# Kernel tuning notes

Measured on AMD Instinct MI355X. Metric: run time of the kernel, lower is better.

The kernel has to match this reference:

```python
import jax, jax.numpy as jnp
import numpy as np

BATCH, N, M, DIM, HID = 4, 2048, 2048, 128, 128
TB = 64  # target block size (mirrors the torch blocked loop, bounds the ijh intermediate)


def setup_inputs() -> dict:
    key = jax.random.key(0)
    k0, k1, k2, k3, k4, k5 = jax.random.split(key, 6)
    s_in = 1.0 / np.sqrt(DIM)
    s_out = 1.0 / np.sqrt(HID)
    return {
        "target_val": jax.random.normal(k0, (BATCH, N, DIM), jnp.float32),
        "source_val": jax.random.normal(k1, (BATCH, M, DIM), jnp.float32),
        "W_in": jax.random.uniform(k2, (HID, DIM), jnp.float32, -s_in, s_in),
        "b_in": jax.random.uniform(k3, (HID,), jnp.float32, -s_in, s_in),
        "W_out": jax.random.uniform(k4, (1, HID), jnp.float32, -s_out, s_out),
        "b_out": jax.random.uniform(k5, (1,), jnp.float32, -s_out, s_out),
    }


def reference(target_val, source_val, W_in, b_in, W_out, b_out):
    # out[b,i,j] = W_out @ silu(W_in @ (t_i * s_j) + b_in) + b_out
    B, Nt, d = target_val.shape
    nb = Nt // TB
    w_out = W_out[0]  # [HID]
    # [nb, B, TB, d] so we can scan over target blocks without materializing [B,N,M,HID]
    t_blocks = target_val.reshape(B, nb, TB, d).transpose(1, 0, 2, 3)

    def block_fn(t_chunk):  # t_chunk: [B, TB, d]
        hidden = jnp.einsum('bid,hd,bjd->bijh', t_chunk, W_in, source_val)  # [B,TB,M,HID]
        hidden = jax.nn.silu(hidden + b_in)
        return jnp.einsum('bijh,h->bij', hidden, w_out) + b_out[0]  # [B,TB,M]

    out_blocks = jax.lax.map(block_fn, t_blocks)  # [nb, B, TB, M]
    return out_blocks.transpose(1, 0, 2, 3).reshape(B, Nt, M)
```

## Files before the change

### kernel.cpp

```cpp
#include <hip/hip_runtime.h>

#define BATCH 4
#define NN 2048
#define MM 2048
#define DIM 128
#define HID 128

typedef __bf16 bf16x8 __attribute__((ext_vector_type(8)));
typedef float f32x16 __attribute__((ext_vector_type(16)));
typedef float f32x4 __attribute__((ext_vector_type(4)));
typedef float f32x2 __attribute__((ext_vector_type(2)));
typedef unsigned short ushort_t;
typedef ushort_t ushort8 __attribute__((ext_vector_type(8)));
typedef unsigned int uint_t;

#define LOG2E 1.44269504088896340736f
#define LN2   0.69314718055994530942f

__device__ __forceinline__ ushort_t f2bf(float f) {
  uint_t u = __builtin_bit_cast(uint_t, f);
  u += 0x7fffu + ((u >> 16) & 1u);
  return (ushort_t)(u >> 16);
}
__device__ __forceinline__ float bflo(uint_t p) { return __builtin_bit_cast(float, p << 16); }
__device__ __forceinline__ float bfhi(uint_t p) { return __builtin_bit_cast(float, p & 0xffff0000u); }

__global__ void cvt_repack(const float* __restrict__ src, ushort_t* __restrict__ dst) {
  int t = blockIdx.x * 256 + threadIdx.x;
  int c    = t & 63;
  int ks   = (t >> 6) & 7;
  int jt   = (t >> 9) & 63;
  int b    = t >> 15;
  int half = c >> 5, l5 = c & 31;
  int j    = jt * 32 + l5;
  int d0   = ks * 16 + half * 8;
  const float* s = src + ((size_t)(b * MM + j)) * DIM + d0;
  float4 v0 = *reinterpret_cast<const float4*>(s);
  float4 v1 = *reinterpret_cast<const float4*>(s + 4);
  ushort8 u;
  u[0] = f2bf(v0.x); u[1] = f2bf(v0.y); u[2] = f2bf(v0.z); u[3] = f2bf(v0.w);
  u[4] = f2bf(v1.x); u[5] = f2bf(v1.y); u[6] = f2bf(v1.z); u[7] = f2bf(v1.w);
  *reinterpret_cast<ushort8*>(dst + (size_t)t * 8) = u;
}

__global__ void pbw_kernel(const float* __restrict__ b_in, const float* __restrict__ w_out,
                           uint_t* __restrict__ pbw) {
  int h = threadIdx.x;
  pbw[h] = (uint_t)f2bf(b_in[h] * LOG2E) | ((uint_t)f2bf(w_out[h] * LN2) << 16);
}

__launch_bounds__(256, 4)
__global__ void hmlp_kernel(const float* __restrict__ Tg, const ushort_t* __restrict__ Sb,
                            const float* __restrict__ Wg, const uint_t* __restrict__ pbw,
                            const float* __restrict__ b_out_p, float* __restrict__ Og) {
  __shared__ float part[4][1024];
  __shared__ ushort_t Bst[2][4096];
  const int tid  = threadIdx.x;
  const int lane = tid & 63;
  const int wv   = tid >> 6;
  const int half = lane >> 5;
  const int l5   = lane & 31;
  const int blk  = blockIdx.x;
  const int b    = blk >> 11;
  const int i    = blk & 2047;
  const int hb   = wv << 5;

  f32x16 cinit;
  uint_t wp[8];
#pragma unroll
  for (int r = 0; r < 16; ++r) {
    uint_t pw = pbw[hb + (r & 3) + 8 * (r >> 2) + 4 * half];
    cinit[r] = bflo(pw);
    if (r & 1) wp[r >> 1] |= (pw & 0xffff0000u);
    else       wp[r >> 1]  = (pw >> 16);
  }

  bf16x8 afr[8];
  {
    const float* tb = Tg + ((size_t)(b * NN + i)) * DIM;
    const float* wr = Wg + (size_t)(hb + l5) * DIM;
#pragma unroll
    for (int ks = 0; ks < 8; ++ks) {
      const int d0 = ks * 16 + half * 8;
      float4 w0 = *reinterpret_cast<const float4*>(wr + d0);
      float4 w1 = *reinterpret_cast<const float4*>(wr + d0 + 4);
      float4 t0 = *reinterpret_cast<const float4*>(tb + d0);
      float4 t1 = *reinterpret_cast<const float4*>(tb + d0 + 4);
      ushort8 u;
      u[0] = f2bf(w0.x * t0.x * LOG2E); u[1] = f2bf(w0.y * t0.y * LOG2E);
      u[2] = f2bf(w0.z * t0.z * LOG2E); u[3] = f2bf(w0.w * t0.w * LOG2E);
      u[4] = f2bf(w1.x * t1.x * LOG2E); u[5] = f2bf(w1.y * t1.y * LOG2E);
      u[6] = f2bf(w1.z * t1.z * LOG2E); u[7] = f2bf(w1.w * t1.w * LOG2E);
      afr[ks] = __builtin_bit_cast(bf16x8, u);
    }
  }

  const ushort_t* stage_base = Sb + (size_t)b * (64 * 4096);

  auto stage_async = [&](int jt, int buf) {
    const ushort_t* g0 = stage_base + (size_t)jt * 4096 + wv * 1024 + lane * 8;
    ushort_t* l0 = &Bst[buf][wv * 1024];
    __builtin_amdgcn_global_load_lds(
        (const __attribute__((address_space(1))) uint_t*)(g0),
        (__attribute__((address_space(3))) uint_t*)(l0), 16, 0, 0);
    __builtin_amdgcn_global_load_lds(
        (const __attribute__((address_space(1))) uint_t*)(g0 + 512),
        (__attribute__((address_space(3))) uint_t*)(l0 + 512), 16, 0, 0);
  };

  const float bo = b_out_p[0];
  const size_t ob = ((size_t)(b * NN + i)) * MM;

  stage_async(0, 0);
  __syncthreads();

#pragma unroll 1
  for (int jt = 0; jt < 64; ++jt) {
    const int buf = jt & 1;
    if (jt + 1 < 64) stage_async(jt + 1, buf ^ 1);

    const ushort_t* fb = &Bst[buf][lane * 8];
    f32x16 c = __builtin_amdgcn_mfma_f32_32x32x16_bf16(
        afr[0], *reinterpret_cast<const bf16x8*>(fb), cinit, 0, 0, 0);
#pragma unroll
    for (int ks = 1; ks < 8; ++ks)
      c = __builtin_amdgcn_mfma_f32_32x32x16_bf16(
          afr[ks], *reinterpret_cast<const bf16x8*>(fb + ks * 512), c, 0, 0, 0);

    f32x2 pc[2] = {f32x2{0.f, 0.f}, f32x2{0.f, 0.f}};
#define EPI_Q(q)                                                                     \
    {                                                                                \
      f32x2 y = __builtin_shufflevector(c, c, 2 * (q), 2 * (q) + 1);                 \
      float e0 = __builtin_amdgcn_exp2f(-y.x);                                       \
      float e1 = __builtin_amdgcn_exp2f(-y.y);                                       \
      f32x2 d = f32x2{e0, e1} + 1.0f;                                                \
      f32x2 s = f32x2{__builtin_amdgcn_rcpf(d.x), __builtin_amdgcn_rcpf(d.y)};       \
      f32x2 ys = y * s;                                                              \
      f32x2 wq = f32x2{bflo(wp[(q)]), bfhi(wp[(q)])};                                \
      pc[(q) & 1] = __builtin_elementwise_fma(wq, ys, pc[(q) & 1]);                  \
    }
    EPI_Q(0) EPI_Q(1) EPI_Q(2) EPI_Q(3) EPI_Q(4) EPI_Q(5) EPI_Q(6) EPI_Q(7)
#undef EPI_Q
    f32x2 pv = pc[0] + pc[1];
    float p = pv.x + pv.y;
    p += __shfl_xor(p, 32, 64);
    if (lane < 32) part[wv][(jt & 31) * 32 + l5] = p;

    __syncthreads();

    if ((jt & 31) == 31) {
      const int phase = jt >> 5;
      const int j0 = tid * 4;
      f32x4 v0 = *reinterpret_cast<const f32x4*>(&part[0][j0]);
      f32x4 v1 = *reinterpret_cast<const f32x4*>(&part[1][j0]);
      f32x4 v2 = *reinterpret_cast<const f32x4*>(&part[2][j0]);
      f32x4 v3 = *reinterpret_cast<const f32x4*>(&part[3][j0]);
      f32x4 o = (v0 + v1) + (v2 + v3);
      o[0] += bo; o[1] += bo; o[2] += bo; o[3] += bo;
      *reinterpret_cast<f32x4*>(&Og[ob + phase * 1024 + j0]) = o;
      __syncthreads();
    }
  }
}

extern "C" void kernel_launch(void* const* d_in, const int* in_sizes, int n_in,
                              void* d_out, int out_size, void* d_ws, size_t ws_size,
                              hipStream_t stream) {
  const float* Tg    = (const float*)d_in[0];
  const float* Sg    = (const float*)d_in[1];
  const float* Wg    = (const float*)d_in[2];
  const float* b_in  = (const float*)d_in[3];
  const float* W_out = (const float*)d_in[4];
  const float* b_out = (const float*)d_in[5];
  float* Og = (float*)d_out;

  ushort_t* Sb = (ushort_t*)d_ws;
  uint_t* pbw  = (uint_t*)((char*)d_ws + (size_t)BATCH * MM * DIM * 2);

  cvt_repack<<<(BATCH * MM * DIM) / (256 * 8), 256, 0, stream>>>(Sg, Sb);
  pbw_kernel<<<1, 128, 0, stream>>>(b_in, W_out, pbw);
  hmlp_kernel<<<BATCH * NN, 256, 0, stream>>>(Tg, Sb, Wg, pbw, b_out, Og);
}
```

Before: 732.0 us.

## Software-pipeline MFMA chain of next tile with SiLU epilogue of previous tile

Restructures the per-tile loop into a two-stage pipeline. Each wave issues the MFMA chain for tile j+1 before running the exp/rcp SiLU epilogue for tile j, with two accumulators alternating between the two LDS buffers. The input bias is no longer loaded as the MFMA accumulator init; it is added in the epilogue from packed bf16 registers. The goal is to overlap matrix-core work with the transcendental-heavy epilogue inside a single wave. The cost is a second live 16-float accumulator, some extra adds, and higher register pressure under the 4-blocks-per-CU launch bound.

```diff
diff --git a/kernel.cpp b/kernel.cpp
--- a/kernel.cpp
+++ b/kernel.cpp
@@ -65,14 +65,12 @@
   const int i    = blk & 2047;
   const int hb   = wv << 5;
 
-  f32x16 cinit;
-  uint_t wp[8];
+  uint_t bp[8], wp[8];
 #pragma unroll
   for (int r = 0; r < 16; ++r) {
     uint_t pw = pbw[hb + (r & 3) + 8 * (r >> 2) + 4 * half];
-    cinit[r] = bflo(pw);
-    if (r & 1) wp[r >> 1] |= (pw & 0xffff0000u);
-    else       wp[r >> 1]  = (pw >> 16);
+    if (r & 1) { bp[r >> 1] |= (pw << 16);       wp[r >> 1] |= (pw & 0xffff0000u); }
+    else       { bp[r >> 1]  = (pw & 0xffffu);   wp[r >> 1]  = (pw >> 16); }
   }
 
   bf16x8 afr[8];
@@ -108,29 +106,23 @@
         (__attribute__((address_space(3))) uint_t*)(l0 + 512), 16, 0, 0);
   };
 
-  const float bo = b_out_p[0];
-  const size_t ob = ((size_t)(b * NN + i)) * MM;
-
-  stage_async(0, 0);
-  __syncthreads();
-
-#pragma unroll 1
-  for (int jt = 0; jt < 64; ++jt) {
-    const int buf = jt & 1;
-    if (jt + 1 < 64) stage_async(jt + 1, buf ^ 1);
-
+  auto chain = [&](int buf) -> f32x16 {
     const ushort_t* fb = &Bst[buf][lane * 8];
     f32x16 c = __builtin_amdgcn_mfma_f32_32x32x16_bf16(
-        afr[0], *reinterpret_cast<const bf16x8*>(fb), cinit, 0, 0, 0);
+        afr[0], *reinterpret_cast<const bf16x8*>(fb), (f32x16)(0.f), 0, 0, 0);
 #pragma unroll
     for (int ks = 1; ks < 8; ++ks)
       c = __builtin_amdgcn_mfma_f32_32x32x16_bf16(
           afr[ks], *reinterpret_cast<const bf16x8*>(fb + ks * 512), c, 0, 0, 0);
-
+    return c;
+  };
+
+  auto epi = [&](const f32x16& c, int jtv) {
     f32x2 pc[2] = {f32x2{0.f, 0.f}, f32x2{0.f, 0.f}};
 #define EPI_Q(q)                                                                     \
     {                                                                                \
-      f32x2 y = __builtin_shufflevector(c, c, 2 * (q), 2 * (q) + 1);                 \
+      f32x2 y = __builtin_shufflevector(c, c, 2 * (q), 2 * (q) + 1)                  \
+              + f32x2{bflo(bp[(q)]), bfhi(bp[(q)])};                                 \
       float e0 = __builtin_amdgcn_exp2f(-y.x);                                       \
       float e1 = __builtin_amdgcn_exp2f(-y.y);                                       \
       f32x2 d = f32x2{e0, e1} + 1.0f;                                                \
@@ -144,23 +136,52 @@
     f32x2 pv = pc[0] + pc[1];
     float p = pv.x + pv.y;
     p += __shfl_xor(p, 32, 64);
-    if (lane < 32) part[wv][(jt & 31) * 32 + l5] = p;
-
+    if (lane < 32) part[wv][(jtv & 31) * 32 + l5] = p;
+  };
+
+  const float bo = b_out_p[0];
+  const size_t ob = ((size_t)(b * NN + i)) * MM;
+
+  auto flush = [&](int phase) {
+    const int j0 = tid * 4;
+    f32x4 v0 = *reinterpret_cast<const f32x4*>(&part[0][j0]);
+    f32x4 v1 = *reinterpret_cast<const f32x4*>(&part[1][j0]);
+    f32x4 v2 = *reinterpret_cast<const f32x4*>(&part[2][j0]);
+    f32x4 v3 = *reinterpret_cast<const f32x4*>(&part[3][j0]);
+    f32x4 o = (v0 + v1) + (v2 + v3);
+    o[0] += bo; o[1] += bo; o[2] += bo; o[3] += bo;
+    *reinterpret_cast<f32x4*>(&Og[ob + phase * 1024 + j0]) = o;
+  };
+
+  stage_async(0, 0);
+  __syncthreads();
+  stage_async(1, 1);
+  f32x16 cA = chain(0);
+  f32x16 cB;
+  __syncthreads();
+
+#pragma unroll 1
+  for (int jt = 1; jt < 63; jt += 2) {
+    stage_async(jt + 1, 0);
+    cB = chain(1);
+    epi(cA, jt - 1);
     __syncthreads();
 
+    if (jt + 2 < 64) stage_async(jt + 2, 1);
+    cA = chain(0);
+    epi(cB, jt);
+    __syncthreads();
     if ((jt & 31) == 31) {
-      const int phase = jt >> 5;
-      const int j0 = tid * 4;
-      f32x4 v0 = *reinterpret_cast<const f32x4*>(&part[0][j0]);
-      f32x4 v1 = *reinterpret_cast<const f32x4*>(&part[1][j0]);
-      f32x4 v2 = *reinterpret_cast<const f32x4*>(&part[2][j0]);
-      f32x4 v3 = *reinterpret_cast<const f32x4*>(&part[3][j0]);
-      f32x4 o = (v0 + v1) + (v2 + v3);
-      o[0] += bo; o[1] += bo; o[2] += bo; o[3] += bo;
-      *reinterpret_cast<f32x4*>(&Og[ob + phase * 1024 + j0]) = o;
+      flush(0);
       __syncthreads();
     }
   }
+
+  cB = chain(1);
+  epi(cA, 62);
+  epi(cB, 63);
+  __syncthreads();
+  flush(1);
 }
 
 extern "C" void kernel_launch(void* const* d_in, const int* in_sizes, int n_in,
```

Measured after the change: 730.5 us. Within noise of the previous version (-0.2%).
